# Performance work log

Hardware: AMD Instinct MI355X
Metric: run time of the kernel (lower is better)

## Reference

```python
import jax, jax.numpy as jnp
import numpy as np

TOP_K = 70
TEMPERATURE = 0.1
EPS_NORM = 1e-12  # F.normalize eps
EPS_GUMBEL = 1e-10


def _l2_normalize(x):
    # matches F.normalize(x, dim=-1): x / max(||x||, eps)
    n = jnp.sqrt(jnp.sum(x * x, axis=-1, keepdims=True))
    return x / jnp.maximum(n, EPS_NORM)


def setup_inputs() -> dict:
    key = jax.random.key(0)
    k1, k2, k3, k4 = jax.random.split(key, 4)
    B, N, D, D2 = 1024, 100000, 1024, 1024
    query = jax.random.normal(k1, (B, D), dtype=jnp.float32)
    en_db = jax.random.normal(k2, (N, D), dtype=jnp.float32)
    es_db = jax.random.normal(k3, (N, D2), dtype=jnp.float32)
    noise = jax.random.uniform(k4, (B, TOP_K), dtype=jnp.float32)
    return {"query": query, "en_db": en_db, "es_db": es_db, "noise": noise}


def reference(query, en_db, es_db, noise):
    q_norm = _l2_normalize(query)            # [B, D]
    db_norm = _l2_normalize(en_db)           # [N, D]
    sims = jnp.matmul(q_norm, db_norm.T)     # [B, N]
    k = min(TOP_K, en_db.shape[0])
    topk_sims, topk_idx = jax.lax.top_k(sims, k)      # [B, k] each
    gumbels = -jnp.log(-jnp.log(noise + EPS_GUMBEL) + EPS_GUMBEL)
    logits = (topk_sims + gumbels) / TEMPERATURE
    attn = jax.nn.softmax(logits, axis=1)    # [B, k]
    topk_es = es_db[topk_idx]                # [B, k, D2] gather
    retrieved = jnp.einsum('bk,bkd->bd', attn, topk_es)  # weighted combine
    return retrieved
```

## Files before the change

### kernel.cpp

```cpp
#include <hip/hip_runtime.h>
#include <hip/hip_bf16.h>
#include <cstdint>

#define B_ROWS   1024
#define N_DB     100000
#define N_PAD    100096
#define DIM      1024
#define TOPK     70
#define CAND_MAX 1024
#define SURV_MAX 256
#define S_Q      508.0f
#define INV_SS   (1.0f / (508.0f * 508.0f))
#define T_CAND   0.0815f
#define FILT_MARGIN 4.5e-3f
#define W_SKIP   1e-5f

typedef int   i32x4 __attribute__((ext_vector_type(4)));
typedef float f32x4 __attribute__((ext_vector_type(4)));

__device__ __forceinline__ void gload_lds16(const void* g, void* l) {
    __builtin_amdgcn_global_load_lds(
        (const __attribute__((address_space(1))) unsigned int*)g,
        (__attribute__((address_space(3))) unsigned int*)l, 16, 0, 0);
}

__global__ void prep_all(const float* __restrict__ query,
                         const float* __restrict__ en_db,
                         signed char* __restrict__ q_i8,
                         signed char* __restrict__ db_i8,
                         double* __restrict__ q_inv,
                         double* __restrict__ db_inv,
                         int* __restrict__ cand_cnt) {
    const int bid = blockIdx.x;
    const int t = threadIdx.x;
    const float* src;
    signed char* dst;
    double* inv;
    int valid;
    if (bid < N_PAD) {
        src = en_db + (size_t)bid * DIM;
        dst = db_i8 + (size_t)bid * DIM;
        inv = db_inv + bid;
        valid = (bid < N_DB);
    } else {
        const int row = bid - N_PAD;
        src = query + (size_t)row * DIM;
        dst = q_i8 + (size_t)row * DIM;
        inv = q_inv + row;
        valid = 1;
        if (t == 0) cand_cnt[row] = 0;
    }
    __shared__ double s_part[4];
    __shared__ double s_inv;
    if (valid) {
        float4 v = ((const float4*)src)[t];
        double acc = (double)v.x * v.x + (double)v.y * v.y +
                     (double)v.z * v.z + (double)v.w * v.w;
        #pragma unroll
        for (int off = 32; off > 0; off >>= 1) acc += __shfl_down(acc, off);
        if ((t & 63) == 0) s_part[t >> 6] = acc;
        __syncthreads();
        if (t == 0) {
            double nn = sqrt(s_part[0] + s_part[1] + s_part[2] + s_part[3]);
            if (nn < 1e-12) nn = 1e-12;
            double iv = 1.0 / nn;
            s_inv = iv;
            *inv = iv;
        }
        __syncthreads();
        const float iv = (float)s_inv * S_Q;
        int qx = (int)rintf(v.x * iv);
        int qy = (int)rintf(v.y * iv);
        int qz = (int)rintf(v.z * iv);
        int qw = (int)rintf(v.w * iv);
        qx = max(-127, min(127, qx));
        qy = max(-127, min(127, qy));
        qz = max(-127, min(127, qz));
        qw = max(-127, min(127, qw));
        char4 o;
        o.x = (signed char)qx; o.y = (signed char)qy;
        o.z = (signed char)qz; o.w = (signed char)qw;
        ((char4*)dst)[t] = o;
    } else {
        char4 z; z.x = z.y = z.z = z.w = 0;
        ((char4*)dst)[t] = z;
        if (t == 0) *inv = 0.0;
    }
}

__launch_bounds__(256, 2)
__global__ void approx_topk_gemm(const signed char* __restrict__ Aq,
                                 const signed char* __restrict__ Bq,
                                 int* __restrict__ cand_cnt,
                                 int* __restrict__ cand_idx,
                                 float* __restrict__ cand_val) {
    __shared__ signed char At[128 * 128];
    __shared__ signed char Bt[128 * 128];
    const int t    = threadIdx.x;
    const int lane = t & 63;
    const int w    = t >> 6;
    const int wr   = w >> 1, wc = w & 1;
    const int r16  = lane & 15, kq = lane >> 4;

    const int d   = blockIdx.x;
    const int lid = (d & 7) * 782 + (d >> 3);
    const int by  = lid >> 3;
    const int bx  = lid & 7;
    const int brow0 = bx * 128;
    const int bcol0 = by * 128;

    i32x4 acc[4][4];
    #pragma unroll
    for (int m = 0; m < 4; ++m)
        #pragma unroll
        for (int n = 0; n < 4; ++n)
            acc[m][n] = (i32x4){0, 0, 0, 0};

    for (int kt = 0; kt < DIM / 128; ++kt) {
        #pragma unroll
        for (int i = 0; i < 4; ++i) {
            const int flat = i * 256 + t;
            const int row  = flat >> 3;
            const int phys = flat & 7;
            const int s    = phys ^ (row & 7);
            gload_lds16(Aq + (size_t)(brow0 + row) * DIM + kt * 128 + s * 16,
                        &At[row * 128 + phys * 16]);
            gload_lds16(Bq + (size_t)(bcol0 + row) * DIM + kt * 128 + s * 16,
                        &Bt[row * 128 + phys * 16]);
        }
        __syncthreads();
        #pragma unroll
        for (int kk = 0; kk < 2; ++kk) {
            i32x4 af[4], bfr[4];
            #pragma unroll
            for (int m = 0; m < 4; ++m) {
                const int row = wr * 64 + m * 16 + r16;
                const int ps  = ((kk << 2) | kq) ^ (row & 7);
                af[m] = *(const i32x4*)&At[row * 128 + ps * 16];
            }
            #pragma unroll
            for (int n = 0; n < 4; ++n) {
                const int row = wc * 64 + n * 16 + r16;
                const int ps  = ((kk << 2) | kq) ^ (row & 7);
                bfr[n] = *(const i32x4*)&Bt[row * 128 + ps * 16];
            }
            #pragma unroll
            for (int m = 0; m < 4; ++m)
                #pragma unroll
                for (int n = 0; n < 4; ++n)
                    acc[m][n] = __builtin_amdgcn_mfma_i32_16x16x64_i8(af[m], bfr[n], acc[m][n], 0, 0, 0);
        }
        __syncthreads();
    }

    #pragma unroll
    for (int m = 0; m < 4; ++m) {
        #pragma unroll
        for (int n = 0; n < 4; ++n) {
            const int c = bcol0 + wc * 64 + n * 16 + r16;
            #pragma unroll
            for (int reg = 0; reg < 4; ++reg) {
                float v = (float)acc[m][n][reg] * INV_SS;
                if (v >= T_CAND && c < N_DB) {
                    int r = brow0 + wr * 64 + m * 16 + kq * 4 + reg;
                    int pos = atomicAdd(&cand_cnt[r], 1);
                    if (pos < CAND_MAX) {
                        cand_idx[r * CAND_MAX + pos] = c;
                        cand_val[r * CAND_MAX + pos] = v;
                    }
                }
            }
        }
    }
}

__launch_bounds__(512)
__global__ void refine_finalize(const float* __restrict__ query,
                                const float* __restrict__ en_db,
                                const float* __restrict__ es_db,
                                const float* __restrict__ noise,
                                const double* __restrict__ q_inv,
                                const double* __restrict__ db_inv,
                                const int* __restrict__ cand_cnt,
                                const int* __restrict__ cand_idx,
                                const float* __restrict__ cand_val,
                                float* __restrict__ out) {
    __shared__ int    hist[256];
    __shared__ int    sL;
    __shared__ int    s_thrbin;
    __shared__ int    s_si[SURV_MAX];
    __shared__ double s_sim[SURV_MAX];
    __shared__ int    s_idx[SURV_MAX];
    __shared__ double s_logit[TOPK];
    __shared__ int    s_top[TOPK];
    __shared__ float  s_wc[TOPK];
    __shared__ int    s_ic[TOPK];
    __shared__ int    s_nk;
    const int b = blockIdx.x;
    const int t = threadIdx.x;
    const int lane = t & 63;
    const int wid  = t >> 6;
    const int cnt = min(cand_cnt[b], CAND_MAX);

    const float4* qg = (const float4*)(query + (size_t)b * DIM);
    float4 qr[4];
    #pragma unroll
    for (int j = 0; j < 4; ++j) qr[j] = qg[j * 64 + lane];
    const double qi = q_inv[b];

    if (t < 256) {
        hist[t] = 0;
        s_sim[t] = -1e300;
        s_idx[t] = 0x7fffffff;
    }
    if (t == 0) sL = 0;
    __syncthreads();
    for (int i = t; i < cnt; i += 512) {
        float v = cand_val[b * CAND_MAX + i];
        int bin = (int)((v - T_CAND) * 1000.0f);
        bin = max(0, min(255, bin));
        atomicAdd(&hist[bin], 1);
    }
    __syncthreads();
    if (t == 0) {
        int acc = 0, bsel = 0;
        for (int k = 255; k >= 0; --k) {
            acc += hist[k];
            if (acc >= TOPK) { bsel = k; break; }
        }
        s_thrbin = bsel;
    }
    __syncthreads();
    const float thr = (T_CAND + s_thrbin * 0.001f) - FILT_MARGIN;
    for (int i = t; i < cnt; i += 512) {
        float v = cand_val[b * CAND_MAX + i];
        if (v >= thr) {
            int p = atomicAdd(&sL, 1);
            if (p < SURV_MAX) s_si[p] = cand_idx[b * CAND_MAX + i];
        }
    }
    __syncthreads();
    const int L = min(sL, SURV_MAX);

    for (int c = wid; c < L; c += 8) {
        const int idx = s_si[c];
        const float4* dv = (const float4*)(en_db + (size_t)idx * DIM);
        double acc = 0.0;
        #pragma unroll
        for (int j = 0; j < 4; ++j) {
            float4 x = dv[j * 64 + lane];
            float4 q = qr[j];
            acc += (double)x.x * q.x + (double)x.y * q.y +
                   (double)x.z * q.z + (double)x.w * q.w;
        }
        #pragma unroll
        for (int off = 32; off > 0; off >>= 1) acc += __shfl_down(acc, off);
        if (lane == 0) {
            s_sim[c] = acc * qi * db_inv[idx];
            s_idx[c] = idx;
        }
    }
    __syncthreads();

    for (int k = 2; k <= SURV_MAX; k <<= 1) {
        for (int j = k >> 1; j > 0; j >>= 1) {
            if (t < SURV_MAX) {
                int i = t;
                int l = i ^ j;
                if (l > i) {
                    double a = s_sim[i], c = s_sim[l];
                    int ia = s_idx[i], ic = s_idx[l];
                    bool iAfter = (a < c) || (a == c && ia > ic);
                    bool lAfter = (c < a) || (c == a && ic > ia);
                    bool dosw = (((i & k) == 0) ? iAfter : lAfter);
                    if (dosw) {
                        s_sim[i] = c; s_sim[l] = a;
                        s_idx[i] = ic; s_idx[l] = ia;
                    }
                }
            }
            __syncthreads();
        }
    }
    if (t < TOPK) {
        double sim = s_sim[t];
        double u = (double)noise[b * TOPK + t];
        double g = -log(-log(u + 1e-10) + 1e-10);
        s_logit[t] = (sim + g) / 0.1;
        s_top[t] = s_idx[t];
    }
    __syncthreads();
    if (t == 0) {
        double mx = -1e300;
        for (int k = 0; k < TOPK; ++k) mx = fmax(mx, s_logit[k]);
        double sum = 0.0;
        for (int k = 0; k < TOPK; ++k) {
            double ev = exp(s_logit[k] - mx);
            s_logit[k] = ev;
            sum += ev;
        }
        double isum = 1.0 / sum;
        int nk = 0;
        for (int k = 0; k < TOPK; ++k) {
            float w = (float)(s_logit[k] * isum);
            if (w >= W_SKIP) {
                s_wc[nk] = w;
                s_ic[nk] = s_top[k];
                ++nk;
            }
        }
        s_nk = nk;
    }
    __syncthreads();
    const int nk = s_nk;
    float2 accv = {0.f, 0.f};
    for (int k = 0; k < nk; ++k) {
        int idx = s_ic[k];
        if (idx < N_DB) {
            float2 v = ((const float2*)(es_db + (size_t)idx * DIM))[t];
            float wk = s_wc[k];
            accv.x += wk * v.x;
            accv.y += wk * v.y;
        }
    }
    ((float2*)(out + (size_t)b * DIM))[t] = accv;
}

extern "C" void kernel_launch(void* const* d_in, const int* in_sizes, int n_in,
                              void* d_out, int out_size, void* d_ws, size_t ws_size,
                              hipStream_t stream) {
    const float* query = (const float*)d_in[0];
    const float* en_db = (const float*)d_in[1];
    const float* es_db = (const float*)d_in[2];
    const float* noise = (const float*)d_in[3];
    float* out = (float*)d_out;

    char* ws = (char*)d_ws;
    size_t off = 0;
    signed char* db_i8 = (signed char*)(ws + off); off += (size_t)N_PAD * DIM;
    double* db_inv     = (double*)(ws + off);      off += (size_t)N_PAD * 8;
    signed char* q_i8  = (signed char*)(ws + off); off += (size_t)B_ROWS * DIM;
    double* q_inv      = (double*)(ws + off);      off += (size_t)B_ROWS * 8;
    int* cand_cnt      = (int*)(ws + off);         off += (size_t)B_ROWS * 4;
    int* cand_idx      = (int*)(ws + off);         off += (size_t)B_ROWS * CAND_MAX * 4;
    float* cand_val    = (float*)(ws + off);       off += (size_t)B_ROWS * CAND_MAX * 4;

    prep_all<<<N_PAD + B_ROWS, 256, 0, stream>>>(query, en_db, q_i8, db_i8,
                                                 q_inv, db_inv, cand_cnt);

    approx_topk_gemm<<<8 * 782, 256, 0, stream>>>(q_i8, db_i8, cand_cnt, cand_idx, cand_val);

    refine_finalize<<<B_ROWS, 512, 0, stream>>>(query, en_db, es_db, noise,
                                                q_inv, db_inv,
                                                cand_cnt, cand_idx, cand_val, out);
}
```

Before: 427.6 us.

## Rewrite int8 candidate GEMM as 256x256 tile with multi-stage LDS pipeline

```diff
diff --git a/kernel.cpp b/kernel.cpp
--- a/kernel.cpp
+++ b/kernel.cpp
@@ -9,10 +9,10 @@
 #define TOPK     70
 #define CAND_MAX 1024
 #define SURV_MAX 256
-#define S_Q      508.0f
-#define INV_SS   (1.0f / (508.0f * 508.0f))
+#define S_Q      677.0f
+#define INV_SS   (1.0f / (677.0f * 677.0f))
 #define T_CAND   0.0815f
-#define FILT_MARGIN 4.5e-3f
+#define FILT_MARGIN 3.5e-3f
 #define W_SKIP   1e-5f
 
 typedef int   i32x4 __attribute__((ext_vector_type(4)));
@@ -88,81 +88,222 @@
     }
 }
 
-__launch_bounds__(256, 2)
+
+#define LDSOFF(buf, op, kh) ((buf)*65536 + (op)*32768 + (kh)*16384)
+
+__device__ __forceinline__ int swz4(int row) {
+    return (row & 3) ^ ((row >> 2) & 3);
+}
+
+__device__ __forceinline__ void stage_unit(const signed char* __restrict__ base,
+                                           int grow0, int kbase,
+                                           signed char* lds_region, int tid) {
+    #pragma unroll
+    for (int r = 0; r < 2; ++r) {
+        const int flat = r * 512 + tid;
+        const int row  = flat >> 2;
+        const int phys = flat & 3;
+        const int s    = phys ^ swz4(row);
+        gload_lds16(base + (size_t)(grow0 + row) * DIM + kbase + s * 16,
+                    lds_region + flat * 16);
+    }
+}
+
+__device__ __forceinline__ void ld_afrag(const signed char* lds, int off, int mh,
+                                         int wr, int r16, int kq, i32x4 (&af)[4]) {
+    #pragma unroll
+    for (int m = 0; m < 4; ++m) {
+        const int row = wr * 128 + mh * 64 + m * 16 + r16;
+        const int ps  = kq ^ swz4(row);
+        af[m] = *(const i32x4*)&lds[off + row * 64 + ps * 16];
+    }
+}
+
+__device__ __forceinline__ void ld_bfrag(const signed char* lds, int off,
+                                         int wc, int r16, int kq, i32x4 (&bfr)[4]) {
+    #pragma unroll
+    for (int n = 0; n < 4; ++n) {
+        const int row = wc * 64 + n * 16 + r16;
+        const int ps  = kq ^ swz4(row);
+        bfr[n] = *(const i32x4*)&lds[off + row * 64 + ps * 16];
+    }
+}
+
+__device__ __forceinline__ void mfma16(i32x4 (&af)[4], i32x4 (&bfr)[4], int mh,
+                                       i32x4 (&acc)[8][4]) {
+    __builtin_amdgcn_s_setprio(1);
+    #pragma unroll
+    for (int m = 0; m < 4; ++m)
+        #pragma unroll
+        for (int n = 0; n < 4; ++n)
+            acc[mh * 4 + m][n] = __builtin_amdgcn_mfma_i32_16x16x64_i8(
+                af[m], bfr[n], acc[mh * 4 + m][n], 0, 0, 0);
+    __builtin_amdgcn_s_setprio(0);
+}
+
+template<int LAST>
+__device__ __forceinline__ void do_iter(const signed char* __restrict__ Aq,
+                                        const signed char* __restrict__ Bq,
+                                        signed char* lds, int t2,
+                                        int brow0, int bcol0, int tid,
+                                        int wr, int wc, int r16, int kq,
+                                        i32x4 (&acc)[8][4]) {
+    i32x4 bfr[4];
+    {
+        i32x4 af[4];
+        ld_bfrag(lds, LDSOFF(0,1,0), wc, r16, kq, bfr);
+        ld_afrag(lds, LDSOFF(0,0,0), 0, wr, r16, kq, af);
+        __builtin_amdgcn_sched_barrier(0);
+        stage_unit(Aq, brow0, (t2+1)*128 + 64, lds + LDSOFF(1,0,1), tid);
+        __builtin_amdgcn_s_barrier();
+        asm volatile("s_waitcnt lgkmcnt(0)" ::: "memory");
+        __builtin_amdgcn_sched_barrier(0);
+        mfma16(af, bfr, 0, acc);
+        __builtin_amdgcn_s_barrier();
+    }
+    {
+        i32x4 af[4];
+        ld_afrag(lds, LDSOFF(0,0,0), 1, wr, r16, kq, af);
+        __builtin_amdgcn_sched_barrier(0);
+        stage_unit(Bq, bcol0, (t2+1)*128 + 64, lds + LDSOFF(1,1,1), tid);
+        __builtin_amdgcn_s_barrier();
+        asm volatile("s_waitcnt lgkmcnt(0)" ::: "memory");
+        __builtin_amdgcn_sched_barrier(0);
+        mfma16(af, bfr, 1, acc);
+        asm volatile("s_waitcnt vmcnt(8)" ::: "memory");
+        __builtin_amdgcn_s_barrier();
+    }
+    {
+        i32x4 af[4];
+        ld_bfrag(lds, LDSOFF(0,1,1), wc, r16, kq, bfr);
+        ld_afrag(lds, LDSOFF(0,0,1), 0, wr, r16, kq, af);
+        __builtin_amdgcn_sched_barrier(0);
+        if constexpr (!LAST) stage_unit(Aq, brow0, (t2+2)*128, lds + LDSOFF(0,0,0), tid);
+        __builtin_amdgcn_s_barrier();
+        asm volatile("s_waitcnt lgkmcnt(0)" ::: "memory");
+        __builtin_amdgcn_sched_barrier(0);
+        mfma16(af, bfr, 0, acc);
+        __builtin_amdgcn_s_barrier();
+    }
+    {
+        i32x4 af[4];
+        ld_afrag(lds, LDSOFF(0,0,1), 1, wr, r16, kq, af);
+        __builtin_amdgcn_sched_barrier(0);
+        if constexpr (!LAST) stage_unit(Bq, bcol0, (t2+2)*128, lds + LDSOFF(0,1,0), tid);
+        __builtin_amdgcn_s_barrier();
+        asm volatile("s_waitcnt lgkmcnt(0)" ::: "memory");
+        __builtin_amdgcn_sched_barrier(0);
+        mfma16(af, bfr, 1, acc);
+        if constexpr (LAST) asm volatile("s_waitcnt vmcnt(4)" ::: "memory");
+        else                asm volatile("s_waitcnt vmcnt(8)" ::: "memory");
+        __builtin_amdgcn_s_barrier();
+    }
+    {
+        i32x4 af[4];
+        ld_bfrag(lds, LDSOFF(1,1,0), wc, r16, kq, bfr);
+        ld_afrag(lds, LDSOFF(1,0,0), 0, wr, r16, kq, af);
+        __builtin_amdgcn_sched_barrier(0);
+        if constexpr (!LAST) stage_unit(Aq, brow0, (t2+2)*128 + 64, lds + LDSOFF(0,0,1), tid);
+        __builtin_amdgcn_s_barrier();
+        asm volatile("s_waitcnt lgkmcnt(0)" ::: "memory");
+        __builtin_amdgcn_sched_barrier(0);
+        mfma16(af, bfr, 0, acc);
+        __builtin_amdgcn_s_barrier();
+    }
+    {
+        i32x4 af[4];
+        ld_afrag(lds, LDSOFF(1,0,0), 1, wr, r16, kq, af);
+        __builtin_amdgcn_sched_barrier(0);
+        if constexpr (!LAST) stage_unit(Bq, bcol0, (t2+2)*128 + 64, lds + LDSOFF(0,1,1), tid);
+        __builtin_amdgcn_s_barrier();
+        asm volatile("s_waitcnt lgkmcnt(0)" ::: "memory");
+        __builtin_amdgcn_sched_barrier(0);
+        mfma16(af, bfr, 1, acc);
+        if constexpr (LAST) asm volatile("s_waitcnt vmcnt(0)" ::: "memory");
+        else                asm volatile("s_waitcnt vmcnt(8)" ::: "memory");
+        __builtin_amdgcn_s_barrier();
+    }
+    {
+        i32x4 af[4];
+        ld_bfrag(lds, LDSOFF(1,1,1), wc, r16, kq, bfr);
+        ld_afrag(lds, LDSOFF(1,0,1), 0, wr, r16, kq, af);
+        __builtin_amdgcn_sched_barrier(0);
+        if constexpr (!LAST) stage_unit(Aq, brow0, (t2+3)*128, lds + LDSOFF(1,0,0), tid);
+        __builtin_amdgcn_s_barrier();
+        asm volatile("s_waitcnt lgkmcnt(0)" ::: "memory");
+        __builtin_amdgcn_sched_barrier(0);
+        mfma16(af, bfr, 0, acc);
+        __builtin_amdgcn_s_barrier();
+    }
+    {
+        i32x4 af[4];
+        ld_afrag(lds, LDSOFF(1,0,1), 1, wr, r16, kq, af);
+        __builtin_amdgcn_sched_barrier(0);
+        if constexpr (!LAST) stage_unit(Bq, bcol0, (t2+3)*128, lds + LDSOFF(1,1,0), tid);
+        __builtin_amdgcn_s_barrier();
+        asm volatile("s_waitcnt lgkmcnt(0)" ::: "memory");
+        __builtin_amdgcn_sched_barrier(0);
+        mfma16(af, bfr, 1, acc);
+        if constexpr (!LAST) {
+            asm volatile("s_waitcnt vmcnt(8)" ::: "memory");
+            __builtin_amdgcn_s_barrier();
+        }
+    }
+}
+
+__launch_bounds__(512, 2)
 __global__ void approx_topk_gemm(const signed char* __restrict__ Aq,
                                  const signed char* __restrict__ Bq,
                                  int* __restrict__ cand_cnt,
                                  int* __restrict__ cand_idx,
                                  float* __restrict__ cand_val) {
-    __shared__ signed char At[128 * 128];
-    __shared__ signed char Bt[128 * 128];
-    const int t    = threadIdx.x;
-    const int lane = t & 63;
-    const int w    = t >> 6;
-    const int wr   = w >> 1, wc = w & 1;
+    extern __shared__ signed char lds[];
+    const int tid  = threadIdx.x;
+    const int lane = tid & 63;
+    const int wid  = tid >> 6;
+    const int wr   = wid >> 2;
+    const int wc   = wid & 3;
     const int r16  = lane & 15, kq = lane >> 4;
 
-    const int d   = blockIdx.x;
-    const int lid = (d & 7) * 782 + (d >> 3);
-    const int by  = lid >> 3;
-    const int bx  = lid & 7;
-    const int brow0 = bx * 128;
-    const int bcol0 = by * 128;
-
-    i32x4 acc[4][4];
-    #pragma unroll
-    for (int m = 0; m < 4; ++m)
+    const int orig = blockIdx.x;
+    const int xcd  = orig & 7, ii = orig >> 3;
+    const int wg   = (xcd < 4) ? (xcd * 196 + ii) : (784 + (xcd - 4) * 195 + ii);
+    const int bx   = wg & 3;
+    const int by   = wg >> 2;
+    const int brow0 = bx * 256;
+    const int bcol0 = by * 256;
+
+    i32x4 acc[8][4];
+    #pragma unroll
+    for (int m = 0; m < 8; ++m)
         #pragma unroll
         for (int n = 0; n < 4; ++n)
             acc[m][n] = (i32x4){0, 0, 0, 0};
 
-    for (int kt = 0; kt < DIM / 128; ++kt) {
-        #pragma unroll
-        for (int i = 0; i < 4; ++i) {
-            const int flat = i * 256 + t;
-            const int row  = flat >> 3;
-            const int phys = flat & 7;
-            const int s    = phys ^ (row & 7);
-            gload_lds16(Aq + (size_t)(brow0 + row) * DIM + kt * 128 + s * 16,
-                        &At[row * 128 + phys * 16]);
-            gload_lds16(Bq + (size_t)(bcol0 + row) * DIM + kt * 128 + s * 16,
-                        &Bt[row * 128 + phys * 16]);
-        }
-        __syncthreads();
-        #pragma unroll
-        for (int kk = 0; kk < 2; ++kk) {
-            i32x4 af[4], bfr[4];
-            #pragma unroll
-            for (int m = 0; m < 4; ++m) {
-                const int row = wr * 64 + m * 16 + r16;
-                const int ps  = ((kk << 2) | kq) ^ (row & 7);
-                af[m] = *(const i32x4*)&At[row * 128 + ps * 16];
-            }
-            #pragma unroll
-            for (int n = 0; n < 4; ++n) {
-                const int row = wc * 64 + n * 16 + r16;
-                const int ps  = ((kk << 2) | kq) ^ (row & 7);
-                bfr[n] = *(const i32x4*)&Bt[row * 128 + ps * 16];
-            }
-            #pragma unroll
-            for (int m = 0; m < 4; ++m)
-                #pragma unroll
-                for (int n = 0; n < 4; ++n)
-                    acc[m][n] = __builtin_amdgcn_mfma_i32_16x16x64_i8(af[m], bfr[n], acc[m][n], 0, 0, 0);
-        }
-        __syncthreads();
-    }
-
-    #pragma unroll
-    for (int m = 0; m < 4; ++m) {
+    stage_unit(Aq, brow0, 0,   lds + LDSOFF(0,0,0), tid);
+    stage_unit(Bq, bcol0, 0,   lds + LDSOFF(0,1,0), tid);
+    stage_unit(Aq, brow0, 64,  lds + LDSOFF(0,0,1), tid);
+    stage_unit(Bq, bcol0, 64,  lds + LDSOFF(0,1,1), tid);
+    stage_unit(Aq, brow0, 128, lds + LDSOFF(1,0,0), tid);
+    stage_unit(Bq, bcol0, 128, lds + LDSOFF(1,1,0), tid);
+    asm volatile("s_waitcnt vmcnt(8)" ::: "memory");
+    __builtin_amdgcn_s_barrier();
+
+    do_iter<0>(Aq, Bq, lds, 0, brow0, bcol0, tid, wr, wc, r16, kq, acc);
+    do_iter<0>(Aq, Bq, lds, 2, brow0, bcol0, tid, wr, wc, r16, kq, acc);
+    do_iter<0>(Aq, Bq, lds, 4, brow0, bcol0, tid, wr, wc, r16, kq, acc);
+    do_iter<1>(Aq, Bq, lds, 6, brow0, bcol0, tid, wr, wc, r16, kq, acc);
+
+    #pragma unroll
+    for (int ai = 0; ai < 8; ++ai) {
         #pragma unroll
         for (int n = 0; n < 4; ++n) {
             const int c = bcol0 + wc * 64 + n * 16 + r16;
             #pragma unroll
             for (int reg = 0; reg < 4; ++reg) {
-                float v = (float)acc[m][n][reg] * INV_SS;
+                float v = (float)acc[ai][n][reg] * INV_SS;
                 if (v >= T_CAND && c < N_DB) {
-                    int r = brow0 + wr * 64 + m * 16 + kq * 4 + reg;
+                    int r = brow0 + wr * 128 + ai * 16 + kq * 4 + reg;
                     int pos = atomicAdd(&cand_cnt[r], 1);
                     if (pos < CAND_MAX) {
                         cand_idx[r * CAND_MAX + pos] = c;
@@ -345,10 +486,13 @@
     int* cand_idx      = (int*)(ws + off);         off += (size_t)B_ROWS * CAND_MAX * 4;
     float* cand_val    = (float*)(ws + off);       off += (size_t)B_ROWS * CAND_MAX * 4;
 
+    hipFuncSetAttribute((const void*)approx_topk_gemm,
+                        hipFuncAttributeMaxDynamicSharedMemorySize, 131072);
+
     prep_all<<<N_PAD + B_ROWS, 256, 0, stream>>>(query, en_db, q_i8, db_i8,
                                                  q_inv, db_inv, cand_cnt);
 
-    approx_topk_gemm<<<8 * 782, 256, 0, stream>>>(q_i8, db_i8, cand_cnt, cand_idx, cand_val);
+    approx_topk_gemm<<<1564, 512, 131072, stream>>>(q_i8, db_i8, cand_cnt, cand_idx, cand_val);
 
     refine_finalize<<<B_ROWS, 512, 0, stream>>>(query, en_db, es_db, noise,
                                                 q_inv, db_inv,
```

Result: slower. 543.9 us (+27.2%).
